# Kernel tuning notes

Hardware: AMD Instinct MI355X
Metric: run time of the kernel (lower is better)

The kernel has to match this reference:

```python
import jax, jax.numpy as jnp
import numpy as np

D_MODEL = 1024
SEQ = 4096
BATCH = 4


def _rope_cos_sin(m, d, dtype=jnp.float32):
    # Faithful to source: theta = 10000 ** (-2*(i-1)/d)  (note the i-1, as in the torch code)
    i = jnp.arange(d // 2, dtype=jnp.float32)
    theta = 10000.0 ** (-2.0 * (i - 1.0) / d)          # [d/2]
    ang = jnp.arange(m, dtype=jnp.float32)[:, None] * theta[None, :]  # [m, d/2]
    return jnp.cos(ang).astype(dtype), jnp.sin(ang).astype(dtype)


def _rotate(t, cos, sin):
    # t: [b, m, d]. Equivalent to (t @ R[pos]) with the source's block-diagonal R:
    # out[2i]   =  t[2i]*cos + t[2i+1]*sin
    # out[2i+1] = -t[2i]*sin + t[2i+1]*cos
    b, m, d = t.shape
    t2 = t.reshape(b, m, d // 2, 2)
    e, o = t2[..., 0], t2[..., 1]
    out = jnp.stack([e * cos + o * sin, -e * sin + o * cos], axis=-1)
    return out.reshape(b, m, d)


def setup_inputs() -> dict:
    key = jax.random.key(0)
    kx, kq, kk, kv = jax.random.split(key, 4)
    s = 1.0 / np.sqrt(D_MODEL)
    return {
        "x": jax.random.normal(kx, (BATCH, SEQ, D_MODEL), dtype=jnp.float32),
        "w_q": jax.random.normal(kq, (D_MODEL, D_MODEL), dtype=jnp.float32) * s,
        "w_k": jax.random.normal(kk, (D_MODEL, D_MODEL), dtype=jnp.float32) * s,
        "w_v": jax.random.normal(kv, (D_MODEL, D_MODEL), dtype=jnp.float32) * s,
    }


def reference(x, w_q, w_k, w_v):
    b, m, d = x.shape
    q = x @ w_q.T  # nn.Linear: y = x W^T
    k = x @ w_k.T
    v = x @ w_v.T
    cos, sin = _rope_cos_sin(m, d, x.dtype)
    q_rot = _rotate(q, cos, sin)
    k_rot = _rotate(k, cos, sin)
    # causal scaled dot-product attention (dropout disabled for deterministic reference)
    scale = 1.0 / jnp.sqrt(jnp.asarray(d, x.dtype))
    scores = jnp.einsum('bqd,bkd->bqk', q_rot, k_rot) * scale  # [b, m, m]
    causal = jnp.tril(jnp.ones((m, m), dtype=bool))
    scores = jnp.where(causal[None], scores, jnp.asarray(-jnp.inf, x.dtype))
    weights = jax.nn.softmax(scores, axis=-1)
    return jnp.einsum('bqk,bkd->bqd', weights, v)
```

## Files before the change

kernel.cpp:

```cpp
#include <hip/hip_runtime.h>

#define BATCH 4
#define SEQ 4096
#define DM 1024
#define HALF_D 512
#define NROWS (BATCH * SEQ)
#define NTILES_TRI 2080

typedef _Float16 f16x8 __attribute__((ext_vector_type(8)));
typedef _Float16 f16x4 __attribute__((ext_vector_type(4)));
typedef _Float16 f16x2 __attribute__((ext_vector_type(2)));
typedef float f32x4 __attribute__((ext_vector_type(4)));

__global__ __launch_bounds__(256) void cvt_f32_f16(
    const float* __restrict__ src, _Float16* __restrict__ dst, int n8) {
  int i = blockIdx.x * 256 + threadIdx.x;
  if (i >= n8) return;
  const float4* s = (const float4*)src;
  float4 a = s[2 * i], b = s[2 * i + 1];
  f16x8 h;
  h[0] = (_Float16)a.x; h[1] = (_Float16)a.y;
  h[2] = (_Float16)a.z; h[3] = (_Float16)a.w;
  h[4] = (_Float16)b.x; h[5] = (_Float16)b.y;
  h[6] = (_Float16)b.z; h[7] = (_Float16)b.w;
  *(f16x8*)&dst[8 * i] = h;
}

__global__ __launch_bounds__(256) void rope_apply(_Float16* __restrict__ T) {
  int idx = blockIdx.x * 256 + threadIdx.x;
  int row = idx >> 9;
  int i = idx & 511;
  int pos = row & (SEQ - 1);
  float theta = expf(-0.017988946039016f * ((float)i - 1.0f));
  float ang = (float)pos * theta;
  float c = cosf(ang), s = sinf(ang);
  f16x2 p = ((f16x2*)T)[idx];
  float e = (float)p[0], o = (float)p[1];
  p[0] = (_Float16)(e * c + o * s);
  p[1] = (_Float16)(o * c - e * s);
  ((f16x2*)T)[idx] = p;
}

template <int MODE>
__global__ __launch_bounds__(256) void gemm_nt(
    const _Float16* __restrict__ A, const _Float16* __restrict__ B,
    void* __restrict__ Cv, int K, int lda, int ldb, int ldc,
    long long strideA, long long strideB, long long strideC) {
  int bx = blockIdx.x, by = blockIdx.y, bz = blockIdx.z;
  if (MODE == 1 && bx > by) return;
  A += (size_t)bz * strideA;
  B += (size_t)bz * strideB;

  __shared__ __align__(16) _Float16 sA[64 * 72];
  __shared__ __align__(16) _Float16 sB[64 * 72];

  int tid = threadIdx.x;
  int lane = tid & 63, wave = tid >> 6;
  int wm = (wave & 1) * 32, wn = (wave >> 1) * 32;
  int r16 = lane & 15, quad = lane >> 4;
  int m0 = by * 64, n0 = bx * 64;

  f32x4 acc[2][2] = {};

  int nkt = (MODE == 2) ? (by + 1) : (K >> 6);

  for (int kt = 0; kt < nkt; ++kt) {
#pragma unroll
    for (int it = 0; it < 2; ++it) {
      int chunk = tid + it * 256;
      int row = chunk >> 3, cc = chunk & 7;
      const _Float16* gA;
      if (MODE == 2) {
        gA = A + (size_t)(by * (by + 1) / 2 + kt) * 4096 + row * 64 + cc * 8;
      } else {
        gA = A + (size_t)(m0 + row) * lda + kt * 64 + cc * 8;
      }
      const _Float16* gB = B + (size_t)(n0 + row) * ldb + kt * 64 + cc * 8;
      *(int4*)(&sA[row * 72 + cc * 8]) = *(const int4*)gA;
      *(int4*)(&sB[row * 72 + cc * 8]) = *(const int4*)gB;
    }
    __syncthreads();

    f16x8 af[2][2], bfr[2][2];
#pragma unroll
    for (int mt = 0; mt < 2; ++mt)
#pragma unroll
      for (int ks = 0; ks < 2; ++ks) {
        af[mt][ks] =
            *(const f16x8*)&sA[(wm + mt * 16 + r16) * 72 + ks * 32 + quad * 8];
        bfr[mt][ks] =
            *(const f16x8*)&sB[(wn + mt * 16 + r16) * 72 + ks * 32 + quad * 8];
      }
#pragma unroll
    for (int ks = 0; ks < 2; ++ks)
#pragma unroll
      for (int mt = 0; mt < 2; ++mt)
#pragma unroll
        for (int nt = 0; nt < 2; ++nt)
          acc[mt][nt] = __builtin_amdgcn_mfma_f32_16x16x32_f16(
              af[mt][ks], bfr[nt][ks], acc[mt][nt], 0, 0, 0);
    __syncthreads();
  }

  if (MODE == 0) {
    _Float16* C = (_Float16*)Cv;
#pragma unroll
    for (int mt = 0; mt < 2; ++mt)
#pragma unroll
      for (int nt = 0; nt < 2; ++nt)
#pragma unroll
        for (int r = 0; r < 4; ++r) {
          int grow = m0 + wm + mt * 16 + quad * 4 + r;
          int gcol = n0 + wn + nt * 16 + r16;
          C[(size_t)grow * ldc + gcol] = (_Float16)acc[mt][nt][r];
        }
  } else if (MODE == 1) {
    _Float16* C = (_Float16*)Cv + (size_t)bz * strideC +
                  (size_t)(by * (by + 1) / 2 + bx) * 4096;
#pragma unroll
    for (int mt = 0; mt < 2; ++mt)
#pragma unroll
      for (int nt = 0; nt < 2; ++nt)
#pragma unroll
        for (int r = 0; r < 4; ++r) {
          int lr = wm + mt * 16 + quad * 4 + r;
          int lc = wn + nt * 16 + r16;
          float v = acc[mt][nt][r] * 0.03125f;
          if (n0 + lc > m0 + lr) v = -3.0e4f;
          C[lr * 64 + lc] = (_Float16)v;
        }
  } else if (MODE == 2) {
    float* C = (float*)Cv + (size_t)bz * strideC;
#pragma unroll
    for (int mt = 0; mt < 2; ++mt)
#pragma unroll
      for (int nt = 0; nt < 2; ++nt)
#pragma unroll
        for (int r = 0; r < 4; ++r) {
          int grow = m0 + wm + mt * 16 + quad * 4 + r;
          int gcol = n0 + wn + nt * 16 + r16;
          C[(size_t)grow * ldc + gcol] = acc[mt][nt][r];
        }
  } else {
    _Float16* C = (_Float16*)Cv;
#pragma unroll
    for (int mt = 0; mt < 2; ++mt)
#pragma unroll
      for (int nt = 0; nt < 2; ++nt) {
        int gcol = n0 + wn + nt * 16 + r16;
        int growb = m0 + wm + mt * 16 + quad * 4;
        int b = growb >> 12;
        int m = growb & (SEQ - 1);
        f16x4 t;
#pragma unroll
        for (int r = 0; r < 4; ++r) t[r] = (_Float16)acc[mt][nt][r];
        *(f16x4*)&C[((size_t)b * DM + gcol) * SEQ + m] = t;
      }
  }
}

__global__ __launch_bounds__(256) void softmax_rows(_Float16* __restrict__ Sp) {
  __shared__ float vals[SEQ];
  __shared__ float red[256];
  int row = blockIdx.x;
  int b = row >> 12;
  int q = row & (SEQ - 1);
  int i = q >> 6, r = q & 63;
  _Float16* base = Sp + (size_t)b * ((size_t)NTILES_TRI * 4096) +
                   (size_t)(i * (i + 1) / 2) * 4096 + (size_t)r * 64;
  int tid = threadIdx.x;
  int Kv = q + 1;
  float m = -__builtin_inff();
  for (int k = tid; k < Kv; k += 256) {
    float v = (float)base[(k >> 6) * 4096 + (k & 63)];
    vals[k] = v;
    m = fmaxf(m, v);
  }
  red[tid] = m;
  __syncthreads();
  for (int s = 128; s > 0; s >>= 1) {
    if (tid < s) red[tid] = fmaxf(red[tid], red[tid + s]);
    __syncthreads();
  }
  m = red[0];
  __syncthreads();
  float l = 0.f;
  for (int k = tid; k < Kv; k += 256) {
    float e = expf(vals[k] - m);
    vals[k] = e;
    l += e;
  }
  red[tid] = l;
  __syncthreads();
  for (int s = 128; s > 0; s >>= 1) {
    if (tid < s) red[tid] += red[tid + s];
    __syncthreads();
  }
  float inv = 1.0f / red[0];
  int Kend = (i + 1) * 64;
  for (int k = tid; k < Kend; k += 256) {
    _Float16 p = (k < Kv) ? (_Float16)(vals[k] * inv) : (_Float16)0.f;
    base[(k >> 6) * 4096 + (k & 63)] = p;
  }
}

extern "C" void kernel_launch(void* const* d_in, const int* in_sizes, int n_in,
                              void* d_out, int out_size, void* d_ws,
                              size_t ws_size, hipStream_t stream) {
  const float* x = (const float*)d_in[0];
  const float* wq = (const float*)d_in[1];
  const float* wk = (const float*)d_in[2];
  const float* wv = (const float*)d_in[3];
  float* out = (float*)d_out;

  char* ws = (char*)d_ws;
  _Float16* Sp = (_Float16*)ws;
  _Float16* xh = (_Float16*)ws;
  _Float16* wqh = (_Float16*)(ws + 33554432);
  _Float16* wkh = wqh + (size_t)DM * DM;
  _Float16* wvh = wkh + (size_t)DM * DM;
  _Float16* vth = (_Float16*)(ws + 68157440);
  _Float16* qh = (_Float16*)d_out;
  _Float16* kh = qh + (size_t)NROWS * DM;
  (void)ws_size; (void)in_sizes; (void)n_in; (void)out_size;

  cvt_f32_f16<<<8192, 256, 0, stream>>>(x, xh, NROWS * DM / 8);
  cvt_f32_f16<<<512, 256, 0, stream>>>(wq, wqh, DM * DM / 8);
  cvt_f32_f16<<<512, 256, 0, stream>>>(wk, wkh, DM * DM / 8);
  cvt_f32_f16<<<512, 256, 0, stream>>>(wv, wvh, DM * DM / 8);

  dim3 g0(DM / 64, NROWS / 64, 1);
  gemm_nt<0><<<g0, 256, 0, stream>>>(xh, wqh, qh, DM, DM, DM, DM, 0, 0, 0);
  gemm_nt<0><<<g0, 256, 0, stream>>>(xh, wkh, kh, DM, DM, DM, DM, 0, 0, 0);
  gemm_nt<3><<<g0, 256, 0, stream>>>(xh, wvh, vth, DM, DM, DM, 0, 0, 0, 0);

  rope_apply<<<NROWS * HALF_D / 256, 256, 0, stream>>>(qh);
  rope_apply<<<NROWS * HALF_D / 256, 256, 0, stream>>>(kh);

  gemm_nt<1><<<dim3(SEQ / 64, SEQ / 64, BATCH), 256, 0, stream>>>(
      qh, kh, Sp, DM, DM, DM, 64, (long long)SEQ * DM, (long long)SEQ * DM,
      (long long)NTILES_TRI * 4096);

  softmax_rows<<<NROWS, 256, 0, stream>>>(Sp);

  gemm_nt<2><<<dim3(DM / 64, SEQ / 64, BATCH), 256, 0, stream>>>(
      Sp, vth, out, SEQ, 0, SEQ, DM, (long long)NTILES_TRI * 4096,
      (long long)DM * SEQ, (long long)SEQ * DM);
}
```

Before: 725.4 us.

## Move GEMMs to 128x128 tiles with direct global-to-LDS loads

All GEMMs move from 64x64 tiles to 128x128 tiles, with each wave computing a 64x64 sub-block (4x4 MFMAs). Operands are loaded straight into LDS with global_load_lds, and the padded LDS layout is dropped. The packed triangular score layout becomes 128x128 tiles, and the PV GEMM walks rows in reverse so the longest blocks start first. Softmax now reads and writes 8-wide vectors, uses __expf, and leaves causal masking to the length bound. The goal is more reuse per global load and less instruction overhead. In exchange, register pressure rises and the unpadded LDS rows may cause bank conflicts.

```diff
diff --git a/kernel.cpp b/kernel.cpp
--- a/kernel.cpp
+++ b/kernel.cpp
@@ -5,12 +5,16 @@
 #define DM 1024
 #define HALF_D 512
 #define NROWS (BATCH * SEQ)
-#define NTILES_TRI 2080
+#define NT128 528
+#define TILE_ELE 16384
 
 typedef _Float16 f16x8 __attribute__((ext_vector_type(8)));
 typedef _Float16 f16x4 __attribute__((ext_vector_type(4)));
 typedef _Float16 f16x2 __attribute__((ext_vector_type(2)));
 typedef float f32x4 __attribute__((ext_vector_type(4)));
+
+#define AS1(p) ((const __attribute__((address_space(1))) void*)(p))
+#define AS3(p) ((__attribute__((address_space(3))) void*)(p))
 
 __global__ __launch_bounds__(256) void cvt_f32_f16(
     const float* __restrict__ src, _Float16* __restrict__ dst, int n8) {
@@ -42,118 +46,116 @@
 }
 
 template <int MODE>
-__global__ __launch_bounds__(256) void gemm_nt(
+__global__ __launch_bounds__(256) void gemm128(
     const _Float16* __restrict__ A, const _Float16* __restrict__ B,
     void* __restrict__ Cv, int K, int lda, int ldb, int ldc,
     long long strideA, long long strideB, long long strideC) {
-  int bx = blockIdx.x, by = blockIdx.y, bz = blockIdx.z;
+  int bx = blockIdx.x, bz = blockIdx.z;
+  int by = (MODE == 2) ? (31 - blockIdx.y) : blockIdx.y;
   if (MODE == 1 && bx > by) return;
   A += (size_t)bz * strideA;
   B += (size_t)bz * strideB;
 
-  __shared__ __align__(16) _Float16 sA[64 * 72];
-  __shared__ __align__(16) _Float16 sB[64 * 72];
-
-  int tid = threadIdx.x;
-  int lane = tid & 63, wave = tid >> 6;
-  int wm = (wave & 1) * 32, wn = (wave >> 1) * 32;
-  int r16 = lane & 15, quad = lane >> 4;
-  int m0 = by * 64, n0 = bx * 64;
-
-  f32x4 acc[2][2] = {};
-
-  int nkt = (MODE == 2) ? (by + 1) : (K >> 6);
+  __shared__ __align__(16) _Float16 sA[128 * 64];
+  __shared__ __align__(16) _Float16 sB[128 * 64];
+
+  const int tid = threadIdx.x;
+  const int lane = tid & 63, wave = tid >> 6;
+  const int wm = (wave & 1) * 64, wn = (wave >> 1) * 64;
+  const int r16 = lane & 15, quad = lane >> 4;
+  const int m0 = by * 128, n0 = bx * 128;
+  const int triBase = by * (by + 1) / 2;
+
+  f32x4 acc[4][4] = {};
+
+  const int nkt = (MODE == 2) ? (by + 1) * 2 : (K >> 6);
 
   for (int kt = 0; kt < nkt; ++kt) {
 #pragma unroll
-    for (int it = 0; it < 2; ++it) {
-      int chunk = tid + it * 256;
-      int row = chunk >> 3, cc = chunk & 7;
+    for (int j = 0; j < 4; ++j) {
+      int c = j * 256 + tid;
+      int row = c >> 3, col = c & 7;
       const _Float16* gA;
       if (MODE == 2) {
-        gA = A + (size_t)(by * (by + 1) / 2 + kt) * 4096 + row * 64 + cc * 8;
+        gA = A + (size_t)(triBase + (kt >> 1)) * TILE_ELE + row * 128 +
+             (kt & 1) * 64 + col * 8;
       } else {
-        gA = A + (size_t)(m0 + row) * lda + kt * 64 + cc * 8;
+        gA = A + (size_t)(m0 + row) * lda + kt * 64 + col * 8;
       }
-      const _Float16* gB = B + (size_t)(n0 + row) * ldb + kt * 64 + cc * 8;
-      *(int4*)(&sA[row * 72 + cc * 8]) = *(const int4*)gA;
-      *(int4*)(&sB[row * 72 + cc * 8]) = *(const int4*)gB;
-    }
-    __syncthreads();
-
-    f16x8 af[2][2], bfr[2][2];
-#pragma unroll
-    for (int mt = 0; mt < 2; ++mt)
-#pragma unroll
-      for (int ks = 0; ks < 2; ++ks) {
-        af[mt][ks] =
-            *(const f16x8*)&sA[(wm + mt * 16 + r16) * 72 + ks * 32 + quad * 8];
-        bfr[mt][ks] =
-            *(const f16x8*)&sB[(wn + mt * 16 + r16) * 72 + ks * 32 + quad * 8];
+      const _Float16* gB = B + (size_t)(n0 + row) * ldb + kt * 64 + col * 8;
+      __builtin_amdgcn_global_load_lds(AS1(gA), AS3(&sA[(j * 256 + wave * 64) * 8]), 16, 0, 0);
+      __builtin_amdgcn_global_load_lds(AS1(gB), AS3(&sB[(j * 256 + wave * 64) * 8]), 16, 0, 0);
+    }
+    __syncthreads();
+
+#pragma unroll
+    for (int ks = 0; ks < 2; ++ks) {
+      f16x8 af[4], bf[4];
+#pragma unroll
+      for (int i = 0; i < 4; ++i) {
+        af[i] = *(const f16x8*)&sA[(wm + i * 16 + r16) * 64 + ks * 32 + quad * 8];
+        bf[i] = *(const f16x8*)&sB[(wn + i * 16 + r16) * 64 + ks * 32 + quad * 8];
       }
 #pragma unroll
-    for (int ks = 0; ks < 2; ++ks)
-#pragma unroll
-      for (int mt = 0; mt < 2; ++mt)
-#pragma unroll
-        for (int nt = 0; nt < 2; ++nt)
-          acc[mt][nt] = __builtin_amdgcn_mfma_f32_16x16x32_f16(
-              af[mt][ks], bfr[nt][ks], acc[mt][nt], 0, 0, 0);
+      for (int mi = 0; mi < 4; ++mi)
+#pragma unroll
+        for (int ni = 0; ni < 4; ++ni)
+          acc[mi][ni] = __builtin_amdgcn_mfma_f32_16x16x32_f16(
+              af[mi], bf[ni], acc[mi][ni], 0, 0, 0);
+    }
     __syncthreads();
   }
 
   if (MODE == 0) {
     _Float16* C = (_Float16*)Cv;
 #pragma unroll
-    for (int mt = 0; mt < 2; ++mt)
-#pragma unroll
-      for (int nt = 0; nt < 2; ++nt)
+    for (int mi = 0; mi < 4; ++mi)
+#pragma unroll
+      for (int ni = 0; ni < 4; ++ni)
 #pragma unroll
         for (int r = 0; r < 4; ++r) {
-          int grow = m0 + wm + mt * 16 + quad * 4 + r;
-          int gcol = n0 + wn + nt * 16 + r16;
-          C[(size_t)grow * ldc + gcol] = (_Float16)acc[mt][nt][r];
+          int grow = m0 + wm + mi * 16 + quad * 4 + r;
+          int gcol = n0 + wn + ni * 16 + r16;
+          C[(size_t)grow * ldc + gcol] = (_Float16)acc[mi][ni][r];
         }
   } else if (MODE == 1) {
     _Float16* C = (_Float16*)Cv + (size_t)bz * strideC +
-                  (size_t)(by * (by + 1) / 2 + bx) * 4096;
-#pragma unroll
-    for (int mt = 0; mt < 2; ++mt)
-#pragma unroll
-      for (int nt = 0; nt < 2; ++nt)
+                  (size_t)(triBase + bx) * TILE_ELE;
+#pragma unroll
+    for (int mi = 0; mi < 4; ++mi)
+#pragma unroll
+      for (int ni = 0; ni < 4; ++ni)
 #pragma unroll
         for (int r = 0; r < 4; ++r) {
-          int lr = wm + mt * 16 + quad * 4 + r;
-          int lc = wn + nt * 16 + r16;
-          float v = acc[mt][nt][r] * 0.03125f;
-          if (n0 + lc > m0 + lr) v = -3.0e4f;
-          C[lr * 64 + lc] = (_Float16)v;
+          int lr = wm + mi * 16 + quad * 4 + r;
+          int lc = wn + ni * 16 + r16;
+          C[lr * 128 + lc] = (_Float16)(acc[mi][ni][r] * 0.03125f);
         }
   } else if (MODE == 2) {
     float* C = (float*)Cv + (size_t)bz * strideC;
 #pragma unroll
-    for (int mt = 0; mt < 2; ++mt)
-#pragma unroll
-      for (int nt = 0; nt < 2; ++nt)
+    for (int mi = 0; mi < 4; ++mi)
+#pragma unroll
+      for (int ni = 0; ni < 4; ++ni)
 #pragma unroll
         for (int r = 0; r < 4; ++r) {
-          int grow = m0 + wm + mt * 16 + quad * 4 + r;
-          int gcol = n0 + wn + nt * 16 + r16;
-          C[(size_t)grow * ldc + gcol] = acc[mt][nt][r];
+          int grow = m0 + wm + mi * 16 + quad * 4 + r;
+          int gcol = n0 + wn + ni * 16 + r16;
+          C[(size_t)grow * ldc + gcol] = acc[mi][ni][r];
         }
   } else {
     _Float16* C = (_Float16*)Cv;
 #pragma unroll
-    for (int mt = 0; mt < 2; ++mt)
-#pragma unroll
-      for (int nt = 0; nt < 2; ++nt) {
-        int gcol = n0 + wn + nt * 16 + r16;
-        int growb = m0 + wm + mt * 16 + quad * 4;
+    for (int mi = 0; mi < 4; ++mi)
+#pragma unroll
+      for (int ni = 0; ni < 4; ++ni) {
+        int gcol = n0 + wn + ni * 16 + r16;
+        int growb = m0 + wm + mi * 16 + quad * 4;
         int b = growb >> 12;
         int m = growb & (SEQ - 1);
         f16x4 t;
 #pragma unroll
-        for (int r = 0; r < 4; ++r) t[r] = (_Float16)acc[mt][nt][r];
+        for (int r = 0; r < 4; ++r) t[r] = (_Float16)acc[mi][ni][r];
         *(f16x4*)&C[((size_t)b * DM + gcol) * SEQ + m] = t;
       }
   }
@@ -165,16 +167,27 @@
   int row = blockIdx.x;
   int b = row >> 12;
   int q = row & (SEQ - 1);
-  int i = q >> 6, r = q & 63;
-  _Float16* base = Sp + (size_t)b * ((size_t)NTILES_TRI * 4096) +
-                   (size_t)(i * (i + 1) / 2) * 4096 + (size_t)r * 64;
+  int i = q >> 7, r = q & 127;
+  _Float16* base = Sp + (size_t)b * ((size_t)NT128 * TILE_ELE) +
+                   (size_t)(i * (i + 1) / 2) * TILE_ELE + (size_t)r * 128;
   int tid = threadIdx.x;
   int Kv = q + 1;
   float m = -__builtin_inff();
-  for (int k = tid; k < Kv; k += 256) {
-    float v = (float)base[(k >> 6) * 4096 + (k & 63)];
-    vals[k] = v;
-    m = fmaxf(m, v);
+  for (int kb = tid * 8; kb + 8 <= Kv; kb += 2048) {
+    f16x8 v8 = *(const f16x8*)&base[(kb >> 7) * TILE_ELE + (kb & 127)];
+#pragma unroll
+    for (int t = 0; t < 8; ++t) {
+      float v = (float)v8[t];
+      vals[kb + t] = v;
+      m = fmaxf(m, v);
+    }
+  }
+  if (tid == 0) {
+    for (int k = Kv & ~7; k < Kv; ++k) {
+      float v = (float)base[(k >> 7) * TILE_ELE + (k & 127)];
+      vals[k] = v;
+      m = fmaxf(m, v);
+    }
   }
   red[tid] = m;
   __syncthreads();
@@ -186,7 +199,7 @@
   __syncthreads();
   float l = 0.f;
   for (int k = tid; k < Kv; k += 256) {
-    float e = expf(vals[k] - m);
+    float e = __expf(vals[k] - m);
     vals[k] = e;
     l += e;
   }
@@ -197,10 +210,15 @@
     __syncthreads();
   }
   float inv = 1.0f / red[0];
-  int Kend = (i + 1) * 64;
-  for (int k = tid; k < Kend; k += 256) {
-    _Float16 p = (k < Kv) ? (_Float16)(vals[k] * inv) : (_Float16)0.f;
-    base[(k >> 6) * 4096 + (k & 63)] = p;
+  int Kend = (i + 1) * 128;
+  for (int kb = tid * 8; kb < Kend; kb += 2048) {
+    f16x8 p;
+#pragma unroll
+    for (int t = 0; t < 8; ++t) {
+      int k = kb + t;
+      p[t] = (k < Kv) ? (_Float16)(vals[k] * inv) : (_Float16)0.f;
+    }
+    *(f16x8*)&base[(kb >> 7) * TILE_ELE + (kb & 127)] = p;
   }
 }
 
@@ -219,7 +237,7 @@
   _Float16* wqh = (_Float16*)(ws + 33554432);
   _Float16* wkh = wqh + (size_t)DM * DM;
   _Float16* wvh = wkh + (size_t)DM * DM;
-  _Float16* vth = (_Float16*)(ws + 68157440);
+  _Float16* vth = (_Float16*)(ws + 69206016);
   _Float16* qh = (_Float16*)d_out;
   _Float16* kh = qh + (size_t)NROWS * DM;
   (void)ws_size; (void)in_sizes; (void)n_in; (void)out_size;
@@ -229,21 +247,21 @@
   cvt_f32_f16<<<512, 256, 0, stream>>>(wk, wkh, DM * DM / 8);
   cvt_f32_f16<<<512, 256, 0, stream>>>(wv, wvh, DM * DM / 8);
 
-  dim3 g0(DM / 64, NROWS / 64, 1);
-  gemm_nt<0><<<g0, 256, 0, stream>>>(xh, wqh, qh, DM, DM, DM, DM, 0, 0, 0);
-  gemm_nt<0><<<g0, 256, 0, stream>>>(xh, wkh, kh, DM, DM, DM, DM, 0, 0, 0);
-  gemm_nt<3><<<g0, 256, 0, stream>>>(xh, wvh, vth, DM, DM, DM, 0, 0, 0, 0);
+  dim3 g0(DM / 128, NROWS / 128, 1);
+  gemm128<0><<<g0, 256, 0, stream>>>(xh, wqh, qh, DM, DM, DM, DM, 0, 0, 0);
+  gemm128<0><<<g0, 256, 0, stream>>>(xh, wkh, kh, DM, DM, DM, DM, 0, 0, 0);
+  gemm128<3><<<g0, 256, 0, stream>>>(xh, wvh, vth, DM, DM, DM, 0, 0, 0, 0);
 
   rope_apply<<<NROWS * HALF_D / 256, 256, 0, stream>>>(qh);
   rope_apply<<<NROWS * HALF_D / 256, 256, 0, stream>>>(kh);
 
-  gemm_nt<1><<<dim3(SEQ / 64, SEQ / 64, BATCH), 256, 0, stream>>>(
-      qh, kh, Sp, DM, DM, DM, 64, (long long)SEQ * DM, (long long)SEQ * DM,
-      (long long)NTILES_TRI * 4096);
+  gemm128<1><<<dim3(SEQ / 128, SEQ / 128, BATCH), 256, 0, stream>>>(
+      qh, kh, Sp, DM, DM, DM, 128, (long long)SEQ * DM, (long long)SEQ * DM,
+      (long long)NT128 * TILE_ELE);
 
   softmax_rows<<<NROWS, 256, 0, stream>>>(Sp);
 
-  gemm_nt<2><<<dim3(DM / 64, SEQ / 64, BATCH), 256, 0, stream>>>(
-      Sp, vth, out, SEQ, 0, SEQ, DM, (long long)NTILES_TRI * 4096,
+  gemm128<2><<<dim3(DM / 128, SEQ / 128, BATCH), 256, 0, stream>>>(
+      Sp, vth, out, SEQ, 0, SEQ, DM, (long long)NT128 * TILE_ELE,
       (long long)DM * SEQ, (long long)SEQ * DM);
 }
```

After: 699.5 us. -3.6%, faster.
